# Optimization experiments

Measured on AMD Instinct MI355X. Metric: run time of the kernel, lower is better.

## Reference

```python
import jax, jax.numpy as jnp
import numpy as np

T = 8388608  # number of timesteps

def setup_inputs() -> dict:
    key = jax.random.key(0)
    x = jax.random.normal(key, (T,), dtype=jnp.float32)
    return {
        "x": x,
        "x0": jnp.float32(0.0),   # initial state estimate
        "p0": jnp.float32(1.0),   # initial covariance
        "A": jnp.float32(0.98),   # state transition
        "H": jnp.float32(1.0),    # observation model
        "Q": jnp.float32(0.01),   # process noise
        "R": jnp.float32(0.1),    # observation noise
    }

def reference(x, x0, p0, A, H, Q, R):
    # Scalar Kalman filter recurrence over T timesteps, expressed as lax.scan.
    def step(carry, y):
        xs, ps = carry
        x_pred = A * xs
        P_pred = A * ps * A + Q
        K = P_pred * H / (H * P_pred * H + R)
        x_new = x_pred + K * (y - H * x_pred)
        p_new = P_pred - K * H * P_pred
        return (x_new, p_new), x_new

    _, esti = jax.lax.scan(step, (x0, p0), x)
    return esti.reshape(x.shape[0], 1)  # matches torch reshape(len_sample, -1)
```

## Files before the change

kernel.cpp:

```cpp
#include <hip/hip_runtime.h>


#define T_TOTAL 8388608
#define PRE 128
#define CONV_ITERS 96
#define CHUNK 4096
#define TILE 256
#define NWAVES (T_TOTAL / CHUNK)
#define NBLOCKS (NWAVES / 4)

__global__ __launch_bounds__(256) void kalman_kernel(
    const float* __restrict__ x,
    const float* __restrict__ x0p, const float* __restrict__ p0p,
    const float* __restrict__ Aip, const float* __restrict__ Hip,
    const float* __restrict__ Qip, const float* __restrict__ Rip,
    float* __restrict__ out)
{
  __shared__ float sA[PRE];
  __shared__ float sK[PRE];

  const int lane = threadIdx.x & 63;
  const int wid  = (blockIdx.x << 2) | (threadIdx.x >> 6);

  const float A = Aip[0], H = Hip[0], Q = Qip[0], R = Rip[0];

  float p = p0p[0];
  for (int i = 0; i < CONV_ITERS; ++i) {
    float Pp = A * p * A + Q;
    float K  = Pp * H / (H * Pp * H + R);
    p = Pp - K * H * Pp;
  }
  float PpInf = A * p * A + Q;
  const float kInf = PpInf * H / (H * PpInf * H + R);
  const float aInf = A * (1.0f - kInf * H);

  if (blockIdx.x == 0) {
    if (threadIdx.x == 0) {
      float pp = p0p[0];
      for (int t = 0; t < PRE; ++t) {
        float Pp = A * pp * A + Q;
        float K  = Pp * H / (H * Pp * H + R);
        sA[t] = A * (1.0f - K * H);
        sK[t] = K;
        pp = Pp - K * H * Pp;
      }
    }
    __syncthreads();
  }

  const long chunkStart = (long)wid * CHUNK;
  const bool first = (wid == 0);
  const long start = first ? 0 : (chunkStart - TILE);
  const int nTiles = first ? (CHUNK / TILE) : (CHUNK / TILE + 1);
  const int skipTiles = first ? 0 : 1;
  float carry = first ? x0p[0] : 0.0f;

  #pragma unroll 2
  for (int t = 0; t < nTiles; ++t) {
    const long base = start + (long)t * TILE;
    const float4 y = *(const float4*)(x + base + (lane << 2));

    float a0, a1, a2, a3, k0, k1, k2, k3;
    if (base == 0) {
      const int e = lane << 2;
      a0 = (e + 0 < PRE) ? sA[e + 0] : aInf;
      a1 = (e + 1 < PRE) ? sA[e + 1] : aInf;
      a2 = (e + 2 < PRE) ? sA[e + 2] : aInf;
      a3 = (e + 3 < PRE) ? sA[e + 3] : aInf;
      k0 = (e + 0 < PRE) ? sK[e + 0] : kInf;
      k1 = (e + 1 < PRE) ? sK[e + 1] : kInf;
      k2 = (e + 2 < PRE) ? sK[e + 2] : kInf;
      k3 = (e + 3 < PRE) ? sK[e + 3] : kInf;
    } else {
      a0 = a1 = a2 = a3 = aInf;
      k0 = k1 = k2 = k3 = kInf;
    }

    float Ac = a0;
    float Bc = k0 * y.x;
    Bc = a1 * Bc + k1 * y.y;  Ac = a1 * Ac;
    Bc = a2 * Bc + k2 * y.z;  Ac = a2 * Ac;
    Bc = a3 * Bc + k3 * y.w;  Ac = a3 * Ac;

    float As = Ac, Bs = Bc;
    #pragma unroll
    for (int off = 1; off < 64; off <<= 1) {
      float Au = __shfl_up(As, off);
      float Bu = __shfl_up(Bs, off);
      if (lane >= off) {
        Bs = As * Bu + Bs;
        As = As * Au;
      }
    }

    const float Axp = __shfl_up(As, 1);
    const float Bxp = __shfl_up(Bs, 1);
    const float xin = (lane == 0) ? carry : (Axp * carry + Bxp);

    const float r0 = a0 * xin + k0 * y.x;
    const float r1 = a1 * r0 + k1 * y.y;
    const float r2 = a2 * r1 + k2 * y.z;
    const float r3 = a3 * r2 + k3 * y.w;

    const float cAll = As * carry + Bs;
    carry = __shfl(cAll, 63);

    if (t >= skipTiles) {
      *(float4*)(out + base + (lane << 2)) = make_float4(r0, r1, r2, r3);
    }
  }
}

extern "C" void kernel_launch(void* const* d_in, const int* in_sizes, int n_in,
                              void* d_out, int out_size, void* d_ws, size_t ws_size,
                              hipStream_t stream) {
  const float* x  = (const float*)d_in[0];
  const float* x0 = (const float*)d_in[1];
  const float* p0 = (const float*)d_in[2];
  const float* A  = (const float*)d_in[3];
  const float* H  = (const float*)d_in[4];
  const float* Q  = (const float*)d_in[5];
  const float* R  = (const float*)d_in[6];
  float* out = (float*)d_out;

  kalman_kernel<<<NBLOCKS, 256, 0, stream>>>(x, x0, p0, A, H, Q, R, out);
}
```

Measured before the change: 104.6 us.

## Shrink per-wave chunk, single-pass 16-element scan with 64-step warm-up carry

Each wave now handles 1024 elements in a single pass. Every lane loads 16 contiguous values, so the old sequential tile loop with its 256-element warm-up tile goes away. The incoming carry is estimated by a wave scan over only the preceding 64 samples, and the steady-state gain converges in 40 iterations instead of 96. The initial gain table is now built in parallel, one thread per entry. This is meant to raise parallelism and cut per-wave serial latency, but the shorter warm-up and fewer convergence iterations may reduce accuracy relative to the exact recurrence.

```diff
diff --git a/kernel.cpp b/kernel.cpp
--- a/kernel.cpp
+++ b/kernel.cpp
@@ -2,12 +2,12 @@
 
 
 #define T_TOTAL 8388608
+#define PER_WAVE 1024
+#define WARM 64
+#define NWAVES (T_TOTAL / PER_WAVE)
+#define NBLOCKS (NWAVES / 4)
+#define CONV_ITERS 40
 #define PRE 128
-#define CONV_ITERS 96
-#define CHUNK 4096
-#define TILE 256
-#define NWAVES (T_TOTAL / CHUNK)
-#define NBLOCKS (NWAVES / 4)
 
 __global__ __launch_bounds__(256) void kalman_kernel(
     const float* __restrict__ x,
@@ -16,98 +16,104 @@
     const float* __restrict__ Qip, const float* __restrict__ Rip,
     float* __restrict__ out)
 {
-  __shared__ float sA[PRE];
-  __shared__ float sK[PRE];
-
   const int lane = threadIdx.x & 63;
   const int wid  = (blockIdx.x << 2) | (threadIdx.x >> 6);
+  const long base = (long)wid * PER_WAVE;
+
+  float ys[16];
+  {
+    const float* xp = x + base + (lane << 4);
+    *(float4*)(ys + 0)  = *(const float4*)(xp + 0);
+    *(float4*)(ys + 4)  = *(const float4*)(xp + 4);
+    *(float4*)(ys + 8)  = *(const float4*)(xp + 8);
+    *(float4*)(ys + 12) = *(const float4*)(xp + 12);
+  }
+  float yw = 0.0f;
+  if (wid > 0) yw = x[base - WARM + lane];
 
   const float A = Aip[0], H = Hip[0], Q = Qip[0], R = Rip[0];
 
   float p = p0p[0];
+  #pragma unroll 4
   for (int i = 0; i < CONV_ITERS; ++i) {
     float Pp = A * p * A + Q;
     float K  = Pp * H / (H * Pp * H + R);
     p = Pp - K * H * Pp;
   }
-  float PpInf = A * p * A + Q;
-  const float kInf = PpInf * H / (H * PpInf * H + R);
+  const float PpI  = A * p * A + Q;
+  const float kInf = PpI * H / (H * PpI * H + R);
   const float aInf = A * (1.0f - kInf * H);
 
+  __shared__ float sA[PRE], sK[PRE];
   if (blockIdx.x == 0) {
-    if (threadIdx.x == 0) {
+    if (threadIdx.x < PRE) {
       float pp = p0p[0];
-      for (int t = 0; t < PRE; ++t) {
+      for (int i = 0; i < (int)threadIdx.x; ++i) {
         float Pp = A * pp * A + Q;
         float K  = Pp * H / (H * Pp * H + R);
-        sA[t] = A * (1.0f - K * H);
-        sK[t] = K;
         pp = Pp - K * H * Pp;
       }
+      float Pp = A * pp * A + Q;
+      float K  = Pp * H / (H * Pp * H + R);
+      sA[threadIdx.x] = A * (1.0f - K * H);
+      sK[threadIdx.x] = K;
     }
     __syncthreads();
   }
 
-  const long chunkStart = (long)wid * CHUNK;
-  const bool first = (wid == 0);
-  const long start = first ? 0 : (chunkStart - TILE);
-  const int nTiles = first ? (CHUNK / TILE) : (CHUNK / TILE + 1);
-  const int skipTiles = first ? 0 : 1;
-  float carry = first ? x0p[0] : 0.0f;
+  float carry;
+  if (wid == 0) {
+    carry = x0p[0];
+  } else {
+    float As = aInf, Bs = kInf * yw;
+    #pragma unroll
+    for (int off = 1; off < 64; off <<= 1) {
+      float Au = __shfl_up(As, off);
+      float Bu = __shfl_up(Bs, off);
+      if (lane >= off) { Bs = As * Bu + Bs; As = As * Au; }
+    }
+    carry = __shfl(Bs, 63);
+  }
 
-  #pragma unroll 2
-  for (int t = 0; t < nTiles; ++t) {
-    const long base = start + (long)t * TILE;
-    const float4 y = *(const float4*)(x + base + (lane << 2));
-
-    float a0, a1, a2, a3, k0, k1, k2, k3;
-    if (base == 0) {
-      const int e = lane << 2;
-      a0 = (e + 0 < PRE) ? sA[e + 0] : aInf;
-      a1 = (e + 1 < PRE) ? sA[e + 1] : aInf;
-      a2 = (e + 2 < PRE) ? sA[e + 2] : aInf;
-      a3 = (e + 3 < PRE) ? sA[e + 3] : aInf;
-      k0 = (e + 0 < PRE) ? sK[e + 0] : kInf;
-      k1 = (e + 1 < PRE) ? sK[e + 1] : kInf;
-      k2 = (e + 2 < PRE) ? sK[e + 2] : kInf;
-      k3 = (e + 3 < PRE) ? sK[e + 3] : kInf;
-    } else {
-      a0 = a1 = a2 = a3 = aInf;
-      k0 = k1 = k2 = k3 = kInf;
+  auto run = [&](auto coef) {
+    float Ac = 1.0f, Bc = 0.0f;
+    #pragma unroll
+    for (int j = 0; j < 16; ++j) {
+      float a, k; coef(j, a, k);
+      Bc = a * Bc + k * ys[j];
+      Ac = a * Ac;
     }
-
-    float Ac = a0;
-    float Bc = k0 * y.x;
-    Bc = a1 * Bc + k1 * y.y;  Ac = a1 * Ac;
-    Bc = a2 * Bc + k2 * y.z;  Ac = a2 * Ac;
-    Bc = a3 * Bc + k3 * y.w;  Ac = a3 * Ac;
-
     float As = Ac, Bs = Bc;
     #pragma unroll
     for (int off = 1; off < 64; off <<= 1) {
       float Au = __shfl_up(As, off);
       float Bu = __shfl_up(Bs, off);
-      if (lane >= off) {
-        Bs = As * Bu + Bs;
-        As = As * Au;
-      }
+      if (lane >= off) { Bs = As * Bu + Bs; As = As * Au; }
     }
-
     const float Axp = __shfl_up(As, 1);
     const float Bxp = __shfl_up(Bs, 1);
-    const float xin = (lane == 0) ? carry : (Axp * carry + Bxp);
+    float r = (lane == 0) ? carry : (Axp * carry + Bxp);
+    #pragma unroll
+    for (int j = 0; j < 16; ++j) {
+      float a, k; coef(j, a, k);
+      r = a * r + k * ys[j];
+      ys[j] = r;
+    }
+    float* op = out + base + (lane << 4);
+    *(float4*)(op + 0)  = *(const float4*)(ys + 0);
+    *(float4*)(op + 4)  = *(const float4*)(ys + 4);
+    *(float4*)(op + 8)  = *(const float4*)(ys + 8);
+    *(float4*)(op + 12) = *(const float4*)(ys + 12);
+  };
 
-    const float r0 = a0 * xin + k0 * y.x;
-    const float r1 = a1 * r0 + k1 * y.y;
-    const float r2 = a2 * r1 + k2 * y.z;
-    const float r3 = a3 * r2 + k3 * y.w;
-
-    const float cAll = As * carry + Bs;
-    carry = __shfl(cAll, 63);
-
-    if (t >= skipTiles) {
-      *(float4*)(out + base + (lane << 2)) = make_float4(r0, r1, r2, r3);
-    }
+  if (wid == 0) {
+    run([&](int j, float& a, float& k) {
+      int e = (lane << 4) + j;
+      if (e < PRE) { a = sA[e]; k = sK[e]; }
+      else         { a = aInf;  k = kInf;  }
+    });
+  } else {
+    run([&](int j, float& a, float& k) { a = aInf; k = kInf; });
   }
 }
 
```

After: 100.1 us. 1.05x faster.
